# Kernel optimization log

Hardware: AMD Instinct MI355X
Metric: run time of the kernel (lower is better)

The kernel has to match this reference:

```python
import jax, jax.numpy as jnp
import numpy as np

B, N, D, C, F, T = 8, 2048, 8, 128, 256, 4


def grover_diffusion(n):
    g = np.ones((n, n), np.float32) * (2.0 / n)
    np.fill_diagonal(g, -1.0 + 2.0 / n)
    return g


def build_swap_indices():
    # D-regular circulant graph: neighbors of j are (j +/- 1..D/2) mod N.
    offsets = np.array([-4, -3, -2, -1, 1, 2, 3, 4])
    cols = (np.arange(N)[:, None] + offsets[None, :]) % N          # [N,D]
    A = np.zeros((N, N), np.int32)
    A[np.arange(N)[:, None], cols] = 1
    nb_sorted = np.sort(cols, axis=1)                               # ascending neighbor ids, as np.argwhere gives
    cum = np.cumsum(A, axis=0) - A                                  # exclusive prefix count per column (scan order j=0..N-1)
    swap_a = nb_sorted.astype(np.int32)                             # [N,D]
    swap_b = cum[np.arange(N)[:, None], nb_sorted].astype(np.int32) # [N,D]
    # same graph for every batch element, tiled to match original per-batch indexing
    return (np.broadcast_to(swap_a, (B, N, D)).copy(),
            np.broadcast_to(swap_b, (B, N, D)).copy())


def setup_inputs() -> dict:
    key = jax.random.key(0)
    k1, k2 = jax.random.split(key)
    init_amps = jax.random.normal(k1, (B, N, D, C), dtype=jnp.float32)
    neibs = jax.random.normal(k2, (B, N, F), dtype=jnp.float32)
    coins = jnp.asarray(np.stack([grover_diffusion(D) for _ in range(T)], 0))  # [T,D,D]
    sa, sb = build_swap_indices()
    return {
        "init_amps": init_amps,
        "neibs": neibs,
        "coins": coins,
        "swap_a": jnp.asarray(sa),
        "swap_b": jnp.asarray(sb),
        "time_steps": T,
        "degree": D,
    }


def reference(init_amps, neibs, coins, swap_a, swap_b, time_steps, degree):
    amps = init_amps  # [B,N,D,C]

    def shift(a_i, sa_i, sb_i):
        # a_i: [N,D,C], sa_i/sb_i: [N,D] -> gathered [N,D,C]
        return a_i[sa_i, sb_i]

    gather = jax.vmap(shift)
    for t in range(time_steps):
        # coin step: matmul(amps.permute(0,1,3,2), coin).permute(0,1,3,2)
        a = jnp.einsum('bndc,de->bnec', amps, coins[t])
        # shift step: amps[b,j,n] = a[b, swap_a[b,j,n], swap_b[b,j,n]]
        amps = gather(a, swap_a, swap_b)

    d = jnp.sum(amps * amps, axis=2)                 # [B,N,C]
    quant_neibs = jnp.einsum('bnc,bnf->bcf', d, neibs)  # d^T @ neibs
    return quant_neibs.reshape(-1, quant_neibs.shape[2])  # [B*C, F]
```

## Files before the change

### kernel.cpp

```cpp
#include <hip/hip_runtime.h>

#define Bv 8
#define Nv 2048
#define Dv 8
#define Cv 128
#define Fv 256
#define Tv 4

#define CC    16
#define TILE  64
#define HALO  16
#define LN    96
#define RS    132
#define NT    32

__global__ __launch_bounds__(LN * 4, 4)
void walk_kernel(const float* __restrict__ amps0,
                 const float* __restrict__ coins,
                 const int* __restrict__ swap_a,
                 const int* __restrict__ swap_b,
                 float* __restrict__ dsum)
{
    __shared__ float abuf[LN * RS];

    const int bid  = blockIdx.x;
    const int b    = bid >> 8;
    const int rem  = bid & 255;
    const int tile = rem >> 3;
    const int c0   = (rem & 7) * CC;

    const int tid = threadIdx.x;
    const int ci4 = tid & 3;
    const int nl  = tid >> 2;

    const int n_load_start = tile * TILE - HALO;
    const int ng = (n_load_start + nl) & (Nv - 1);

    float4 amp[Dv];
    int    idx[Dv];

    {
        const float* srcf = amps0 + ((size_t)(b * Nv + ng) * Dv) * Cv + c0 + ci4 * 4;
        #pragma unroll
        for (int dd = 0; dd < Dv; ++dd)
            amp[dd] = *reinterpret_cast<const float4*>(srcf + (size_t)dd * Cv);
    }

    {
        const int* pa = swap_a + (size_t)(b * Nv + ng) * Dv;
        const int* pb = swap_b + (size_t)(b * Nv + ng) * Dv;
        #pragma unroll
        for (int dd = 0; dd < Dv; ++dd) {
            const int sa = pa[dd];
            const int sb = pb[dd];
            int s1 = sa - n_load_start;
            if (s1 < 0)   s1 += Nv;
            if (s1 >= Nv) s1 -= Nv;
            if (s1 >= LN) s1 &= 63;
            idx[dd] = s1 * RS + sb * CC + ci4 * 4;
        }
    }

    float wdv[Tv], wov[Tv];
    bool uni = true;
    #pragma unroll
    for (int tt = 0; tt < Tv; ++tt) {
        const float* cm = coins + tt * Dv * Dv;
        wdv[tt] = cm[0];
        wov[tt] = cm[1];
        #pragma unroll
        for (int i = 0; i < Dv; ++i)
            #pragma unroll
            for (int j = 0; j < Dv; ++j)
                uni = uni && (cm[i * Dv + j] == ((i == j) ? wdv[tt] : wov[tt]));
    }

    #pragma unroll
    for (int t = 0; t < Tv; ++t) {
        float4 a[Dv];
        if (uni) {
            const float wo = wov[t];
            const float dw = wdv[t] - wo;
            float4 s = amp[0];
            #pragma unroll
            for (int dd = 1; dd < Dv; ++dd) {
                s.x += amp[dd].x; s.y += amp[dd].y;
                s.z += amp[dd].z; s.w += amp[dd].w;
            }
            const float4 ws = {wo * s.x, wo * s.y, wo * s.z, wo * s.w};
            #pragma unroll
            for (int e = 0; e < Dv; ++e) {
                a[e].x = fmaf(dw, amp[e].x, ws.x);
                a[e].y = fmaf(dw, amp[e].y, ws.y);
                a[e].z = fmaf(dw, amp[e].z, ws.z);
                a[e].w = fmaf(dw, amp[e].w, ws.w);
            }
        } else {
            const float* cm = coins + t * Dv * Dv;
            #pragma unroll
            for (int e = 0; e < Dv; ++e) { a[e].x = a[e].y = a[e].z = a[e].w = 0.f; }
            #pragma unroll
            for (int dd = 0; dd < Dv; ++dd) {
                #pragma unroll
                for (int e = 0; e < Dv; ++e) {
                    const float w = cm[dd * Dv + e];
                    a[e].x += amp[dd].x * w;
                    a[e].y += amp[dd].y * w;
                    a[e].z += amp[dd].z * w;
                    a[e].w += amp[dd].w * w;
                }
            }
        }

        {
            float* base = abuf + nl * RS + ci4 * 4;
            #pragma unroll
            for (int e = 0; e < Dv; ++e)
                *reinterpret_cast<float4*>(base + e * CC) = a[e];
        }
        __syncthreads();
        #pragma unroll
        for (int dd = 0; dd < Dv; ++dd)
            amp[dd] = *reinterpret_cast<const float4*>(&abuf[idx[dd]]);
        __syncthreads();
    }

    if (nl >= HALO && nl < HALO + TILE) {
        float4 s;
        s.x = s.y = s.z = s.w = 0.f;
        #pragma unroll
        for (int dd = 0; dd < Dv; ++dd) {
            s.x += amp[dd].x * amp[dd].x;
            s.y += amp[dd].y * amp[dd].y;
            s.z += amp[dd].z * amp[dd].z;
            s.w += amp[dd].w * amp[dd].w;
        }
        *reinterpret_cast<float4*>(dsum + (size_t)(b * Nv + ng) * Cv + c0 + ci4 * 4) = s;
    }
}

#define NSPL  8
constexpr size_t OUT_FLOATS = (size_t)Bv * Cv * Fv;
constexpr size_t DSUM_BYTES = (size_t)Bv * Nv * Cv * 4;
constexpr size_t PART_BYTES = (size_t)NSPL * OUT_FLOATS * 4;

typedef float v2f __attribute__((ext_vector_type(2)));

template<int NSPL_>
__global__ __launch_bounds__(256)
void quant_kernel(const float* __restrict__ dsum,
                  const float* __restrict__ neibs,
                  float* __restrict__ dst)
{
    const int bid = blockIdx.x;
    const int nc  = bid % NSPL_;
    int r = bid / NSPL_;
    const int ft = r & 3;  r >>= 2;
    const int ct = r & 1;  r >>= 1;
    const int b  = r;

    const int tid = threadIdx.x;
    const int tf  = tid & 15;
    const int tc  = tid >> 4;

    const int c0  = ct * 64 + tc * 4;
    const int f0  = ft * 64 + tf * 4;
    const int n0  = nc * (Nv / NSPL_);
    const int nch = Nv / NSPL_;

    const float* dg = dsum  + ((size_t)b * Nv + n0) * Cv + c0;
    const float* ng = neibs + ((size_t)b * Nv + n0) * Fv + f0;

    v2f acc[4][2];
    #pragma unroll
    for (int i = 0; i < 4; ++i) {
        acc[i][0] = (v2f){0.f, 0.f};
        acc[i][1] = (v2f){0.f, 0.f};
    }

    #pragma unroll 4
    for (int k = 0; k < nch; ++k) {
        const float4 dv = *reinterpret_cast<const float4*>(dg + (size_t)k * Cv);
        const float4 nv = *reinterpret_cast<const float4*>(ng + (size_t)k * Fv);
        const v2f nb0 = {nv.x, nv.y};
        const v2f nb1 = {nv.z, nv.w};
        acc[0][0] += nb0 * dv.x;  acc[0][1] += nb1 * dv.x;
        acc[1][0] += nb0 * dv.y;  acc[1][1] += nb1 * dv.y;
        acc[2][0] += nb0 * dv.z;  acc[2][1] += nb1 * dv.z;
        acc[3][0] += nb0 * dv.w;  acc[3][1] += nb1 * dv.w;
    }

    float* op = dst + (size_t)nc * OUT_FLOATS + ((size_t)b * Cv + c0) * Fv + f0;
    #pragma unroll
    for (int i = 0; i < 4; ++i) {
        const float4 v = {acc[i][0].x, acc[i][0].y, acc[i][1].x, acc[i][1].y};
        *reinterpret_cast<float4*>(op + (size_t)i * Fv) = v;
    }
}

__global__ __launch_bounds__(256)
void reduce_kernel(const float* __restrict__ partials, float* __restrict__ out)
{
    const size_t i = ((size_t)blockIdx.x * 256 + threadIdx.x) * 4;
    float4 s = {0.f, 0.f, 0.f, 0.f};
    #pragma unroll
    for (int nc = 0; nc < NSPL; ++nc) {
        const float4 p = *reinterpret_cast<const float4*>(partials + nc * OUT_FLOATS + i);
        s.x += p.x; s.y += p.y; s.z += p.z; s.w += p.w;
    }
    *reinterpret_cast<float4*>(out + i) = s;
}

extern "C" void kernel_launch(void* const* d_in, const int* in_sizes, int n_in,
                              void* d_out, int out_size, void* d_ws, size_t ws_size,
                              hipStream_t stream)
{
    const float* amps   = (const float*)d_in[0];
    const float* neibs  = (const float*)d_in[1];
    const float* coins  = (const float*)d_in[2];
    const int*   swap_a = (const int*)d_in[3];
    const int*   swap_b = (const int*)d_in[4];
    float* out  = (float*)d_out;
    float* dsum = (float*)d_ws;

    walk_kernel<<<Bv * NT * (Cv / CC), LN * 4, 0, stream>>>(
        amps, coins, swap_a, swap_b, dsum);

    const bool use_partials = (ws_size >= DSUM_BYTES + PART_BYTES);
    float* partials = (float*)((char*)d_ws + DSUM_BYTES);

    if (use_partials) {
        quant_kernel<NSPL><<<Bv * 2 * 4 * NSPL, 256, 0, stream>>>(dsum, neibs, partials);
        reduce_kernel<<<(int)(OUT_FLOATS / 4 / 256), 256, 0, stream>>>(partials, out);
    } else {
        quant_kernel<1><<<Bv * 2 * 4, 256, 0, stream>>>(dsum, neibs, out);
    }
}
```

Measured before the change: 197.7 us.

## Swizzle walk LDS layout and fuse quant split-K reduction in-block

The walk kernel's shared-memory row stride drops from padded 132 to 128 floats, and an XOR swizzle on row index bits now spreads the float4 stores and gathers across LDS banks. The quant kernel is restructured: each block handles two channels for all 256 features, splits N across four waves, and reduces the partials through shared memory. This replaces the separate partial-sum buffer and reduce kernel, removing one launch and the global partial traffic. In exchange each block reloads all of neibs per channel pair, which adds L2 traffic, and per-thread register tiling is smaller.

```diff
diff --git a/kernel.cpp b/kernel.cpp
--- a/kernel.cpp
+++ b/kernel.cpp
@@ -11,9 +11,8 @@
 #define TILE  64
 #define HALO  16
 #define LN    96
-#define RS    132
+#define RS    128
 #define NT    32
-
 __global__ __launch_bounds__(LN * 4, 4)
 void walk_kernel(const float* __restrict__ amps0,
                  const float* __restrict__ coins,
@@ -57,7 +56,7 @@
             if (s1 < 0)   s1 += Nv;
             if (s1 >= Nv) s1 -= Nv;
             if (s1 >= LN) s1 &= 63;
-            idx[dd] = s1 * RS + sb * CC + ci4 * 4;
+            idx[dd] = s1 * RS + ((sb * CC + ci4 * 4) ^ ((s1 & 7) << 4));
         }
     }
 
@@ -74,6 +73,9 @@
             for (int j = 0; j < Dv; ++j)
                 uni = uni && (cm[i * Dv + j] == ((i == j) ? wdv[tt] : wov[tt]));
     }
+
+    const int rowbase = nl * RS;
+    const int swz     = (nl & 7) << 4;
 
     #pragma unroll
     for (int t = 0; t < Tv; ++t) {
@@ -112,12 +114,9 @@
             }
         }
 
-        {
-            float* base = abuf + nl * RS + ci4 * 4;
-            #pragma unroll
-            for (int e = 0; e < Dv; ++e)
-                *reinterpret_cast<float4*>(base + e * CC) = a[e];
-        }
+        #pragma unroll
+        for (int e = 0; e < Dv; ++e)
+            *reinterpret_cast<float4*>(abuf + rowbase + ((e * CC + ci4 * 4) ^ swz)) = a[e];
         __syncthreads();
         #pragma unroll
         for (int dd = 0; dd < Dv; ++dd)
@@ -139,76 +138,59 @@
     }
 }
 
-#define NSPL  8
-constexpr size_t OUT_FLOATS = (size_t)Bv * Cv * Fv;
-constexpr size_t DSUM_BYTES = (size_t)Bv * Nv * Cv * 4;
-constexpr size_t PART_BYTES = (size_t)NSPL * OUT_FLOATS * 4;
-
-typedef float v2f __attribute__((ext_vector_type(2)));
-
-template<int NSPL_>
 __global__ __launch_bounds__(256)
 void quant_kernel(const float* __restrict__ dsum,
                   const float* __restrict__ neibs,
-                  float* __restrict__ dst)
+                  float* __restrict__ out)
 {
-    const int bid = blockIdx.x;
-    const int nc  = bid % NSPL_;
-    int r = bid / NSPL_;
-    const int ft = r & 3;  r >>= 2;
-    const int ct = r & 1;  r >>= 1;
-    const int b  = r;
-
-    const int tid = threadIdx.x;
-    const int tf  = tid & 15;
-    const int tc  = tid >> 4;
-
-    const int c0  = ct * 64 + tc * 4;
-    const int f0  = ft * 64 + tf * 4;
-    const int n0  = nc * (Nv / NSPL_);
-    const int nch = Nv / NSPL_;
-
-    const float* dg = dsum  + ((size_t)b * Nv + n0) * Cv + c0;
-    const float* ng = neibs + ((size_t)b * Nv + n0) * Fv + f0;
-
-    v2f acc[4][2];
-    #pragma unroll
-    for (int i = 0; i < 4; ++i) {
-        acc[i][0] = (v2f){0.f, 0.f};
-        acc[i][1] = (v2f){0.f, 0.f};
-    }
+    __shared__ float4 sbuf[4][2][64];
+
+    const int bid  = blockIdx.x;
+    const int cp   = bid & 63;
+    const int b    = bid >> 6;
+    const int tid  = threadIdx.x;
+    const int lane = tid & 63;
+    const int w    = tid >> 6;
+    const int c0   = cp * 2;
+
+    const float* dp = dsum  + ((size_t)(b * Nv + w * 512)) * Cv + c0;
+    const float* np = neibs + ((size_t)(b * Nv + w * 512)) * Fv + lane * 4;
+
+    float4 acc0 = {0.f, 0.f, 0.f, 0.f};
+    float4 acc1 = {0.f, 0.f, 0.f, 0.f};
 
     #pragma unroll 4
-    for (int k = 0; k < nch; ++k) {
-        const float4 dv = *reinterpret_cast<const float4*>(dg + (size_t)k * Cv);
-        const float4 nv = *reinterpret_cast<const float4*>(ng + (size_t)k * Fv);
-        const v2f nb0 = {nv.x, nv.y};
-        const v2f nb1 = {nv.z, nv.w};
-        acc[0][0] += nb0 * dv.x;  acc[0][1] += nb1 * dv.x;
-        acc[1][0] += nb0 * dv.y;  acc[1][1] += nb1 * dv.y;
-        acc[2][0] += nb0 * dv.z;  acc[2][1] += nb1 * dv.z;
-        acc[3][0] += nb0 * dv.w;  acc[3][1] += nb1 * dv.w;
-    }
-
-    float* op = dst + (size_t)nc * OUT_FLOATS + ((size_t)b * Cv + c0) * Fv + f0;
-    #pragma unroll
-    for (int i = 0; i < 4; ++i) {
-        const float4 v = {acc[i][0].x, acc[i][0].y, acc[i][1].x, acc[i][1].y};
-        *reinterpret_cast<float4*>(op + (size_t)i * Fv) = v;
-    }
-}
-
-__global__ __launch_bounds__(256)
-void reduce_kernel(const float* __restrict__ partials, float* __restrict__ out)
-{
-    const size_t i = ((size_t)blockIdx.x * 256 + threadIdx.x) * 4;
-    float4 s = {0.f, 0.f, 0.f, 0.f};
-    #pragma unroll
-    for (int nc = 0; nc < NSPL; ++nc) {
-        const float4 p = *reinterpret_cast<const float4*>(partials + nc * OUT_FLOATS + i);
-        s.x += p.x; s.y += p.y; s.z += p.z; s.w += p.w;
-    }
-    *reinterpret_cast<float4*>(out + i) = s;
+    for (int k = 0; k < 512; ++k) {
+        const float2 dv = *reinterpret_cast<const float2*>(dp + (size_t)k * Cv);
+        const float4 nv = *reinterpret_cast<const float4*>(np + (size_t)k * Fv);
+        acc0.x = fmaf(nv.x, dv.x, acc0.x);
+        acc0.y = fmaf(nv.y, dv.x, acc0.y);
+        acc0.z = fmaf(nv.z, dv.x, acc0.z);
+        acc0.w = fmaf(nv.w, dv.x, acc0.w);
+        acc1.x = fmaf(nv.x, dv.y, acc1.x);
+        acc1.y = fmaf(nv.y, dv.y, acc1.y);
+        acc1.z = fmaf(nv.z, dv.y, acc1.z);
+        acc1.w = fmaf(nv.w, dv.y, acc1.w);
+    }
+
+    sbuf[w][0][lane] = acc0;
+    sbuf[w][1][lane] = acc1;
+    __syncthreads();
+
+    if (tid < 128) {
+        const int cc = tid >> 6;
+        const int f4 = tid & 63;
+        const float4 p0 = sbuf[0][cc][f4];
+        const float4 p1 = sbuf[1][cc][f4];
+        const float4 p2 = sbuf[2][cc][f4];
+        const float4 p3 = sbuf[3][cc][f4];
+        float4 s;
+        s.x = (p0.x + p1.x) + (p2.x + p3.x);
+        s.y = (p0.y + p1.y) + (p2.y + p3.y);
+        s.z = (p0.z + p1.z) + (p2.z + p3.z);
+        s.w = (p0.w + p1.w) + (p2.w + p3.w);
+        *reinterpret_cast<float4*>(out + ((size_t)(b * Cv + c0 + cc)) * Fv + f4 * 4) = s;
+    }
 }
 
 extern "C" void kernel_launch(void* const* d_in, const int* in_sizes, int n_in,
@@ -226,13 +208,5 @@
     walk_kernel<<<Bv * NT * (Cv / CC), LN * 4, 0, stream>>>(
         amps, coins, swap_a, swap_b, dsum);
 
-    const bool use_partials = (ws_size >= DSUM_BYTES + PART_BYTES);
-    float* partials = (float*)((char*)d_ws + DSUM_BYTES);
-
-    if (use_partials) {
-        quant_kernel<NSPL><<<Bv * 2 * 4 * NSPL, 256, 0, stream>>>(dsum, neibs, partials);
-        reduce_kernel<<<(int)(OUT_FLOATS / 4 / 256), 256, 0, stream>>>(partials, out);
-    } else {
-        quant_kernel<1><<<Bv * 2 * 4, 256, 0, stream>>>(dsum, neibs, out);
-    }
+    quant_kernel<<<Bv * 64, 256, 0, stream>>>(dsum, neibs, out);
 }
```

After: 229.4 us. 1.16x slower.
